# Optimization experiments

Measured on AMD Instinct MI355X. Metric: run time of the kernel, lower is better.

Reference implementation:

```python
import jax, jax.numpy as jnp
import numpy as np

N, T, K = 400000, 64, 3


def setup_inputs() -> dict:
    key = jax.random.key(0)
    ks = jax.random.split(key, 6)
    G = jax.random.randint(ks[0], (N, 1), 0, 3).astype(jnp.float32)   # genotype 0/1/2
    S = jax.random.randint(ks[1], (N, T, 1), 0, 2).astype(jnp.float32)  # binary exposure
    C = jax.random.uniform(ks[2], (N, T, 1), dtype=jnp.float32)         # cumulative pack-years (scaled)
    Y = (jax.random.uniform(ks[3], (N, T, 1)) < 0.05).astype(jnp.float32)  # rare binary outcome
    L = jax.random.normal(ks[4], (N, K), dtype=jnp.float32)             # covariates
    kw = jax.random.split(ks[5], 2)
    f32 = jnp.float32
    params = dict(
        psi=jnp.array([0.5], f32),
        gamma_S=jnp.array([0.1], f32),
        gamma_C=jnp.array([0.1], f32),
        gamma_G=jnp.array([0.1], f32),
        gamma_GS=jnp.array([0.0], f32),
        gamma_GC=jnp.array([0.0], f32),
        gamma_L_w=jax.random.normal(kw[0], (1, K), f32) * 0.1,
        log_sigma_Z=jnp.array([-2.0], f32),
        beta_0=jnp.array([-3.0], f32),
        beta_Z=jnp.array([0.5], f32),
        beta_S=jnp.array([0.1], f32),
        beta_G=jnp.array([0.1], f32),
        beta_GS=jnp.array([0.0], f32),
        beta_L_w=jax.random.normal(kw[1], (1, K), f32) * 0.1,
    )
    return dict(G=G, S=S, C=C, Y=Y, L=L, **params)


def reference(G, S, C, Y, L, psi, gamma_S, gamma_C, gamma_G, gamma_GS, gamma_GC,
              gamma_L_w, log_sigma_Z, beta_0, beta_Z, beta_S, beta_G, beta_GS, beta_L_w):
    """Faithful JAX port of HiddenMarkovGFormulaV2.forward_filter (fit_interaction=fit_pack_years=True).
    Returns (Z_filtered (N,T,1), Z_variance (N,T,1), log_likelihood scalar)."""
    sigma2 = jnp.exp(log_sigma_Z) ** 2            # sigma_Z^2, shape (1,)
    gL = L @ gamma_L_w.T                          # (N,1) covariate term for transition
    bL = L @ beta_L_w.T                           # (N,1) covariate term for outcome

    def step(carry, xs):
        Z_mean, Z_var = carry                     # each (N,1)
        S_t, C_t, Y_t = xs                        # each (N,1)
        # hidden state transition
        Z_pred = (psi * Z_mean + gamma_S * S_t + gamma_G * G + gamma_C * C_t
                  + gamma_GS * (G * S_t) + gamma_GC * (G * C_t) + gL)
        Z_pred_var = psi ** 2 * Z_var + sigma2
        # outcome probability
        logit = jnp.clip(beta_0 + beta_Z * Z_pred + beta_S * S_t + beta_G * G
                         + beta_GS * (G * S_t) + bL, -20.0, 20.0)
        p = jax.nn.sigmoid(logit)
        # Laplace-style measurement update
        grad = (Y_t - p) * beta_Z
        hess = beta_Z ** 2 * p * (1.0 - p) + 1e-6
        Z_post_var = 1.0 / (1.0 / Z_pred_var + hess)
        Z_post_mean = Z_pred + Z_post_var * grad
        ll = jnp.sum(Y_t * jnp.log(p + 1e-10) + (1.0 - Y_t) * jnp.log(1.0 - p + 1e-10))
        return (Z_post_mean, Z_post_var), (Z_post_mean, Z_post_var, ll)

    n = G.shape[0]
    Zm0 = jnp.zeros((n, 1), dtype=G.dtype)
    Zv0 = jnp.ones((n, 1), dtype=G.dtype)
    xs = (jnp.swapaxes(S, 0, 1), jnp.swapaxes(C, 0, 1), jnp.swapaxes(Y, 0, 1))  # (T,N,1)
    _, (Zf, Zvf, lls) = jax.lax.scan(step, (Zm0, Zv0), xs)
    Z_filtered = jnp.swapaxes(Zf, 0, 1)   # (N,T,1)
    Z_variance = jnp.swapaxes(Zvf, 0, 1)  # (N,T,1)
    return Z_filtered, Z_variance, jnp.sum(lls)
```

## Files before the change

kernel.cpp:

```cpp
#include <hip/hip_runtime.h>


#define TT 64
#define KK 3
#define BT 128
#define WPB (BT / 64)
#define CT 16
#define LDP 66

__global__ __launch_bounds__(256) void ll_reduce_kernel(
    const float* __restrict__ part, float* __restrict__ ll_out, int nb)
{
    float s = 0.0f;
    for (int i = threadIdx.x; i < nb; i += 256) s += part[i];
    #pragma unroll
    for (int off = 32; off > 0; off >>= 1) s += __shfl_down(s, off, 64);
    __shared__ float ws[4];
    const int wid = threadIdx.x >> 6, lane = threadIdx.x & 63;
    if (lane == 0) ws[wid] = s;
    __syncthreads();
    if (threadIdx.x == 0) *ll_out = ws[0] + ws[1] + ws[2] + ws[3];
}

__global__ __launch_bounds__(BT, 4) void hmm_filter_kernel(
    const float* __restrict__ G,
    const float* __restrict__ S,
    const float* __restrict__ C,
    const float* __restrict__ Y,
    const float* __restrict__ L,
    const float* __restrict__ p_psi,
    const float* __restrict__ p_gS,
    const float* __restrict__ p_gC,
    const float* __restrict__ p_gG,
    const float* __restrict__ p_gGS,
    const float* __restrict__ p_gGC,
    const float* __restrict__ p_gLw,
    const float* __restrict__ p_lsZ,
    const float* __restrict__ p_b0,
    const float* __restrict__ p_bZ,
    const float* __restrict__ p_bS,
    const float* __restrict__ p_bG,
    const float* __restrict__ p_bGS,
    const float* __restrict__ p_bLw,
    float* __restrict__ Zf,
    float* __restrict__ Zv,
    float* __restrict__ ll_part,
    int N)
{
    __shared__ float sS [WPB][CT][LDP];
    __shared__ float sCY[WPB][CT][LDP];
    __shared__ float wll[WPB];

    const int tid   = threadIdx.x;
    const int w     = tid >> 6;
    const int l     = tid & 63;
    const int wbase = blockIdx.x * BT + w * 64;
    const int n     = wbase + l;
    const bool valid = (n < N);

    const float psi  = p_psi[0];
    const float gS   = p_gS[0];
    const float gC   = p_gC[0];
    const float gG   = p_gG[0];
    const float gGS  = p_gGS[0];
    const float gGC  = p_gGC[0];
    const float b0   = p_b0[0];
    const float bZ   = p_bZ[0];
    const float bS   = p_bS[0];
    const float bG   = p_bG[0];
    const float bGS  = p_bGS[0];
    const float esz  = expf(p_lsZ[0]);
    const float sigma2 = esz * esz;
    const float psi2 = psi * psi;
    const float bZ2  = bZ * bZ;
    const float gw0 = p_gLw[0], gw1 = p_gLw[1], gw2 = p_gLw[2];
    const float bw0 = p_bLw[0], bw1 = p_bLw[1], bw2 = p_bLw[2];

    float a_s = 0.0f, a_c = 0.0f, zbase = 0.0f, b_s = 0.0f, lbase = 0.0f;
    if (valid) {
        const float Gv = G[n];
        const float l0 = L[n * KK + 0];
        const float l1 = L[n * KK + 1];
        const float l2 = L[n * KK + 2];
        const float gL = l0 * gw0 + l1 * gw1 + l2 * gw2;
        const float bL = l0 * bw0 + l1 * bw1 + l2 * bw2;
        a_s   = gS + gGS * Gv;
        a_c   = gC + gGC * Gv;
        zbase = gG * Gv + gL;
        b_s   = bS + bGS * Gv;
        lbase = b0 + bG * Gv + bL;
    } else {
        lbase = b0;
    }

    float zm  = 0.0f;
    float zv  = 1.0f;
    float ll2 = 0.0f;

    const float4* S4 = (const float4*)S;
    const float4* C4 = (const float4*)C;
    const float4* Y4 = (const float4*)Y;
    float4* Zf4 = (float4*)Zf;
    float4* Zv4 = (float4*)Zv;

    const int rq = l >> 2;
    const int cc = l & 3;
    const int tb = cc * 4;

    float4 rs[4], rc[4], ry[4];

    #pragma unroll
    for (int i = 0; i < 4; ++i) {
        const int nn = wbase + rq + i * 16;
        if (nn < N) {
            const int gidx = nn * (TT / 4) + cc;
            rs[i] = S4[gidx]; rc[i] = C4[gidx]; ry[i] = Y4[gidx];
        } else {
            rs[i] = make_float4(0, 0, 0, 0);
            rc[i] = rs[i]; ry[i] = rs[i];
        }
    }

    for (int t0 = 0; t0 < TT; t0 += CT) {
        #pragma unroll
        for (int i = 0; i < 4; ++i) {
            const int r = rq + i * 16;
            sS[w][tb + 0][r] = rs[i].x; sS[w][tb + 1][r] = rs[i].y;
            sS[w][tb + 2][r] = rs[i].z; sS[w][tb + 3][r] = rs[i].w;
            sCY[w][tb + 0][r] = __uint_as_float(__float_as_uint(rc[i].x) | (__float_as_uint(ry[i].x) << 8));
            sCY[w][tb + 1][r] = __uint_as_float(__float_as_uint(rc[i].y) | (__float_as_uint(ry[i].y) << 8));
            sCY[w][tb + 2][r] = __uint_as_float(__float_as_uint(rc[i].z) | (__float_as_uint(ry[i].z) << 8));
            sCY[w][tb + 3][r] = __uint_as_float(__float_as_uint(rc[i].w) | (__float_as_uint(ry[i].w) << 8));
        }

        if (t0 + CT < TT) {
            const int fo = ((t0 + CT) >> 2) + cc;
            #pragma unroll
            for (int i = 0; i < 4; ++i) {
                const int nn = wbase + rq + i * 16;
                if (nn < N) {
                    const int gidx = nn * (TT / 4) + fo;
                    rs[i] = S4[gidx]; rc[i] = C4[gidx]; ry[i] = Y4[gidx];
                }
            }
        }

        asm volatile("s_waitcnt lgkmcnt(0)" ::: "memory");

        #pragma unroll
        for (int t = 0; t < CT; ++t) {
            const float s      = sS[w][t][l];
            const unsigned cyb = __float_as_uint(sCY[w][t][l]);
            const float c      = __uint_as_float(cyb & 0x7fffffffu);
            const bool  yb     = (cyb >> 31) != 0u;

            const float zpred = fmaf(psi, zm, fmaf(a_s, s, fmaf(a_c, c, zbase)));
            const float zpvar = fmaf(psi2, zv, sigma2);

            float logit = fmaf(bZ, zpred, fmaf(b_s, s, lbase));
            logit = fminf(fmaxf(logit, -20.0f), 20.0f);
            const float p   = __builtin_amdgcn_rcpf(1.0f + __expf(-logit));
            const float omp = 1.0f - p;

            const float ymp = yb ? omp : -p;
            const float sel = yb ? p : omp;

            const float hess = fmaf(bZ2 * p, omp, 1e-6f);
            const float zpostvar  = zpvar * __builtin_amdgcn_rcpf(fmaf(zpvar, hess, 1.0f));
            const float zpostmean = fmaf(zpostvar * bZ, ymp, zpred);

            ll2 += __log2f(sel + 1e-10f);

            zm = zpostmean;
            zv = zpostvar;
            sS [w][t][l] = zpostmean;
            sCY[w][t][l] = zpostvar;
        }

        asm volatile("s_waitcnt lgkmcnt(0)" ::: "memory");

        #pragma unroll
        for (int i = 0; i < 4; ++i) {
            const int r  = rq + i * 16;
            const int nn = wbase + r;
            if (nn < N) {
                float4 vf, vv;
                vf.x = sS [w][tb + 0][r]; vf.y = sS [w][tb + 1][r];
                vf.z = sS [w][tb + 2][r]; vf.w = sS [w][tb + 3][r];
                vv.x = sCY[w][tb + 0][r]; vv.y = sCY[w][tb + 1][r];
                vv.z = sCY[w][tb + 2][r]; vv.w = sCY[w][tb + 3][r];
                const int gidx = nn * (TT / 4) + (t0 >> 2) + cc;
                Zf4[gidx] = vf;
                Zv4[gidx] = vv;
            }
        }
    }

    float ll = valid ? ll2 * 0.69314718055994531f : 0.0f;
    #pragma unroll
    for (int off = 32; off > 0; off >>= 1) {
        ll += __shfl_down(ll, off, 64);
    }
    if (l == 0) wll[w] = ll;
    __syncthreads();
    if (tid == 0) {
        float sacc = 0.0f;
        #pragma unroll
        for (int ww = 0; ww < WPB; ++ww) sacc += wll[ww];
        ll_part[blockIdx.x] = sacc;
    }
}

extern "C" void kernel_launch(void* const* d_in, const int* in_sizes, int n_in,
                              void* d_out, int out_size, void* d_ws, size_t ws_size,
                              hipStream_t stream) {
    const int N = in_sizes[0];

    const float* G   = (const float*)d_in[0];
    const float* S   = (const float*)d_in[1];
    const float* C   = (const float*)d_in[2];
    const float* Y   = (const float*)d_in[3];
    const float* L   = (const float*)d_in[4];
    const float* psi = (const float*)d_in[5];
    const float* gS  = (const float*)d_in[6];
    const float* gC  = (const float*)d_in[7];
    const float* gG  = (const float*)d_in[8];
    const float* gGS = (const float*)d_in[9];
    const float* gGC = (const float*)d_in[10];
    const float* gLw = (const float*)d_in[11];
    const float* lsZ = (const float*)d_in[12];
    const float* b0  = (const float*)d_in[13];
    const float* bZ  = (const float*)d_in[14];
    const float* bS  = (const float*)d_in[15];
    const float* bG  = (const float*)d_in[16];
    const float* bGS = (const float*)d_in[17];
    const float* bLw = (const float*)d_in[18];

    float* out = (float*)d_out;
    float* Zf = out;
    float* Zv = out + (size_t)N * TT;
    float* ll = out + (size_t)2 * N * TT;

    float* ll_part = (float*)d_ws;

    const int blocks = (N + BT - 1) / BT;
    hmm_filter_kernel<<<blocks, BT, 0, stream>>>(
        G, S, C, Y, L, psi, gS, gC, gG, gGS, gGC, gLw, lsZ,
        b0, bZ, bS, bG, bGS, bLw, Zf, Zv, ll_part, N);
    ll_reduce_kernel<<<1, 256, 0, stream>>>(ll_part, ll, blocks);
}
```

Baseline: 505.3 us.

## Replace LDS-staged transposes with per-thread full-row register loads

Drops the shared-memory staging and chunked time loop. Each thread now loads its entire 64-step S/C/Y row into registers, runs the fully unrolled recurrence and writes outputs as float4 rows. The log-likelihood partials are written per wave instead of being reduced per block. This removes LDS traffic and waitcnt barriers, but it makes global accesses uncoalesced across lanes and greatly raises register pressure, which risks spilling and low occupancy.

```diff
diff --git a/kernel.cpp b/kernel.cpp
--- a/kernel.cpp
+++ b/kernel.cpp
@@ -3,16 +3,13 @@
 
 #define TT 64
 #define KK 3
-#define BT 128
-#define WPB (BT / 64)
-#define CT 16
-#define LDP 66
+#define BT 256
 
 __global__ __launch_bounds__(256) void ll_reduce_kernel(
-    const float* __restrict__ part, float* __restrict__ ll_out, int nb)
+    const float* __restrict__ part, float* __restrict__ ll_out, int nw)
 {
     float s = 0.0f;
-    for (int i = threadIdx.x; i < nb; i += 256) s += part[i];
+    for (int i = threadIdx.x; i < nw; i += 256) s += part[i];
     #pragma unroll
     for (int off = 32; off > 0; off >>= 1) s += __shfl_down(s, off, 64);
     __shared__ float ws[4];
@@ -22,7 +19,30 @@
     if (threadIdx.x == 0) *ll_out = ws[0] + ws[1] + ws[2] + ws[3];
 }
 
-__global__ __launch_bounds__(BT, 4) void hmm_filter_kernel(
+#define STEP(SV, CV, YV, OM, OV)                                            \
+    {                                                                       \
+        const float s_  = (SV);                                             \
+        const float c_  = (CV);                                             \
+        const bool  yb_ = ((YV) != 0.0f);                                   \
+        const float zpred = fmaf(psi, zm, fmaf(a_s, s_, fmaf(a_c, c_, zbase))); \
+        const float zpvar = fmaf(psi2, zv, sigma2);                         \
+        float logit = fmaf(bZ, zpred, fmaf(b_s, s_, lbase));                \
+        logit = fminf(fmaxf(logit, -20.0f), 20.0f);                         \
+        const float p_   = __builtin_amdgcn_rcpf(1.0f + __expf(-logit));    \
+        const float omp_ = 1.0f - p_;                                       \
+        const float ymp_ = yb_ ? omp_ : -p_;                                \
+        const float sel_ = yb_ ? p_ : omp_;                                 \
+        const float hess_ = fmaf(bZ2 * p_, omp_, 1e-6f);                    \
+        const float zpostvar_  = zpvar * __builtin_amdgcn_rcpf(fmaf(zpvar, hess_, 1.0f)); \
+        const float zpostmean_ = fmaf(zpostvar_ * bZ, ymp_, zpred);         \
+        ll2 += __log2f(sel_ + 1e-10f);                                      \
+        zm = zpostmean_;                                                    \
+        zv = zpostvar_;                                                     \
+        (OM) = zpostmean_;                                                  \
+        (OV) = zpostvar_;                                                   \
+    }
+
+__global__ __launch_bounds__(BT, 2) void hmm_filter_kernel(
     const float* __restrict__ G,
     const float* __restrict__ S,
     const float* __restrict__ C,
@@ -47,15 +67,8 @@
     float* __restrict__ ll_part,
     int N)
 {
-    __shared__ float sS [WPB][CT][LDP];
-    __shared__ float sCY[WPB][CT][LDP];
-    __shared__ float wll[WPB];
-
-    const int tid   = threadIdx.x;
-    const int w     = tid >> 6;
-    const int l     = tid & 63;
-    const int wbase = blockIdx.x * BT + w * 64;
-    const int n     = wbase + l;
+    const int tid = threadIdx.x;
+    const int n   = blockIdx.x * BT + tid;
     const bool valid = (n < N);
 
     const float psi  = p_psi[0];
@@ -93,107 +106,48 @@
         lbase = b0;
     }
 
-    float zm  = 0.0f;
-    float zv  = 1.0f;
-    float ll2 = 0.0f;
-
     const float4* S4 = (const float4*)S;
     const float4* C4 = (const float4*)C;
     const float4* Y4 = (const float4*)Y;
     float4* Zf4 = (float4*)Zf;
     float4* Zv4 = (float4*)Zv;
-
-    const int rq = l >> 2;
-    const int cc = l & 3;
-    const int tb = cc * 4;
-
-    float4 rs[4], rc[4], ry[4];
-
-    #pragma unroll
-    for (int i = 0; i < 4; ++i) {
-        const int nn = wbase + rq + i * 16;
-        if (nn < N) {
-            const int gidx = nn * (TT / 4) + cc;
-            rs[i] = S4[gidx]; rc[i] = C4[gidx]; ry[i] = Y4[gidx];
-        } else {
+    const int rb = n * (TT / 4);
+
+    float4 rs[TT / 4], rc[TT / 4], ry[TT / 4];
+    if (valid) {
+        #pragma unroll
+        for (int i = 0; i < TT / 4; ++i) {
+            rs[i] = S4[rb + i];
+            rc[i] = C4[rb + i];
+            ry[i] = Y4[rb + i];
+        }
+    } else {
+        #pragma unroll
+        for (int i = 0; i < TT / 4; ++i) {
             rs[i] = make_float4(0, 0, 0, 0);
             rc[i] = rs[i]; ry[i] = rs[i];
         }
     }
-
-    for (int t0 = 0; t0 < TT; t0 += CT) {
-        #pragma unroll
-        for (int i = 0; i < 4; ++i) {
-            const int r = rq + i * 16;
-            sS[w][tb + 0][r] = rs[i].x; sS[w][tb + 1][r] = rs[i].y;
-            sS[w][tb + 2][r] = rs[i].z; sS[w][tb + 3][r] = rs[i].w;
-            sCY[w][tb + 0][r] = __uint_as_float(__float_as_uint(rc[i].x) | (__float_as_uint(ry[i].x) << 8));
-            sCY[w][tb + 1][r] = __uint_as_float(__float_as_uint(rc[i].y) | (__float_as_uint(ry[i].y) << 8));
-            sCY[w][tb + 2][r] = __uint_as_float(__float_as_uint(rc[i].z) | (__float_as_uint(ry[i].z) << 8));
-            sCY[w][tb + 3][r] = __uint_as_float(__float_as_uint(rc[i].w) | (__float_as_uint(ry[i].w) << 8));
-        }
-
-        if (t0 + CT < TT) {
-            const int fo = ((t0 + CT) >> 2) + cc;
-            #pragma unroll
-            for (int i = 0; i < 4; ++i) {
-                const int nn = wbase + rq + i * 16;
-                if (nn < N) {
-                    const int gidx = nn * (TT / 4) + fo;
-                    rs[i] = S4[gidx]; rc[i] = C4[gidx]; ry[i] = Y4[gidx];
-                }
-            }
-        }
-
-        asm volatile("s_waitcnt lgkmcnt(0)" ::: "memory");
-
-        #pragma unroll
-        for (int t = 0; t < CT; ++t) {
-            const float s      = sS[w][t][l];
-            const unsigned cyb = __float_as_uint(sCY[w][t][l]);
-            const float c      = __uint_as_float(cyb & 0x7fffffffu);
-            const bool  yb     = (cyb >> 31) != 0u;
-
-            const float zpred = fmaf(psi, zm, fmaf(a_s, s, fmaf(a_c, c, zbase)));
-            const float zpvar = fmaf(psi2, zv, sigma2);
-
-            float logit = fmaf(bZ, zpred, fmaf(b_s, s, lbase));
-            logit = fminf(fmaxf(logit, -20.0f), 20.0f);
-            const float p   = __builtin_amdgcn_rcpf(1.0f + __expf(-logit));
-            const float omp = 1.0f - p;
-
-            const float ymp = yb ? omp : -p;
-            const float sel = yb ? p : omp;
-
-            const float hess = fmaf(bZ2 * p, omp, 1e-6f);
-            const float zpostvar  = zpvar * __builtin_amdgcn_rcpf(fmaf(zpvar, hess, 1.0f));
-            const float zpostmean = fmaf(zpostvar * bZ, ymp, zpred);
-
-            ll2 += __log2f(sel + 1e-10f);
-
-            zm = zpostmean;
-            zv = zpostvar;
-            sS [w][t][l] = zpostmean;
-            sCY[w][t][l] = zpostvar;
-        }
-
-        asm volatile("s_waitcnt lgkmcnt(0)" ::: "memory");
-
-        #pragma unroll
-        for (int i = 0; i < 4; ++i) {
-            const int r  = rq + i * 16;
-            const int nn = wbase + r;
-            if (nn < N) {
-                float4 vf, vv;
-                vf.x = sS [w][tb + 0][r]; vf.y = sS [w][tb + 1][r];
-                vf.z = sS [w][tb + 2][r]; vf.w = sS [w][tb + 3][r];
-                vv.x = sCY[w][tb + 0][r]; vv.y = sCY[w][tb + 1][r];
-                vv.z = sCY[w][tb + 2][r]; vv.w = sCY[w][tb + 3][r];
-                const int gidx = nn * (TT / 4) + (t0 >> 2) + cc;
-                Zf4[gidx] = vf;
-                Zv4[gidx] = vv;
-            }
-        }
+    __builtin_amdgcn_sched_barrier(0);
+
+    float4 of[TT / 4], ov[TT / 4];
+    float zm  = 0.0f;
+    float zv  = 1.0f;
+    float ll2 = 0.0f;
+
+    #pragma unroll
+    for (int i = 0; i < TT / 4; ++i) {
+        STEP(rs[i].x, rc[i].x, ry[i].x, of[i].x, ov[i].x);
+        STEP(rs[i].y, rc[i].y, ry[i].y, of[i].y, ov[i].y);
+        STEP(rs[i].z, rc[i].z, ry[i].z, of[i].z, ov[i].z);
+        STEP(rs[i].w, rc[i].w, ry[i].w, of[i].w, ov[i].w);
+    }
+
+    if (valid) {
+        #pragma unroll
+        for (int i = 0; i < TT / 4; ++i) Zf4[rb + i] = of[i];
+        #pragma unroll
+        for (int i = 0; i < TT / 4; ++i) Zv4[rb + i] = ov[i];
     }
 
     float ll = valid ? ll2 * 0.69314718055994531f : 0.0f;
@@ -201,13 +155,8 @@
     for (int off = 32; off > 0; off >>= 1) {
         ll += __shfl_down(ll, off, 64);
     }
-    if (l == 0) wll[w] = ll;
-    __syncthreads();
-    if (tid == 0) {
-        float sacc = 0.0f;
-        #pragma unroll
-        for (int ww = 0; ww < WPB; ++ww) sacc += wll[ww];
-        ll_part[blockIdx.x] = sacc;
+    if ((tid & 63) == 0) {
+        ll_part[blockIdx.x * (BT / 64) + (tid >> 6)] = ll;
     }
 }
 
@@ -244,8 +193,9 @@
     float* ll_part = (float*)d_ws;
 
     const int blocks = (N + BT - 1) / BT;
+    const int nwaves = blocks * (BT / 64);
     hmm_filter_kernel<<<blocks, BT, 0, stream>>>(
         G, S, C, Y, L, psi, gS, gC, gG, gGS, gGC, gLw, lsZ,
         b0, bZ, bS, bG, bGS, bLw, Zf, Zv, ll_part, N);
-    ll_reduce_kernel<<<1, 256, 0, stream>>>(ll_part, ll, blocks);
+    ll_reduce_kernel<<<1, 256, 0, stream>>>(ll_part, ll, nwaves);
 }
```

Result: faster. 491.1 us (-2.8%).
